# Optimization experiments

Measured on AMD Instinct MI355X. Metric: run time of the kernel, lower is better.

Reference implementation:

```python
import jax, jax.numpy as jnp
import numpy as np

B, T, C = 4, 2048, 1024
E = 8            # n_expert
K = 2            # n_expert_per_token
H = 1408         # moe_intermediate_size
HS = 1408 * 2    # shared expert intermediate (moe_intermediate_size * n_shared_expert)


def setup_inputs() -> dict:
    key = jax.random.key(0)
    k = jax.random.split(key, 8)
    s = 0.02
    return {
        "x":   jax.random.normal(k[0], (B, T, C), jnp.float32),
        "Wg":  jax.random.normal(k[1], (C, E), jnp.float32) * s,      # router gate
        "W1":  jax.random.normal(k[2], (E, C, H), jnp.float32) * s,   # fc_1 per expert
        "W2":  jax.random.normal(k[3], (E, C, H), jnp.float32) * s,   # fc_2 per expert
        "W3":  jax.random.normal(k[4], (E, H, C), jnp.float32) * s,   # proj per expert
        "Ws1": jax.random.normal(k[5], (C, HS), jnp.float32) * s,     # shared fc_1
        "Ws2": jax.random.normal(k[6], (C, HS), jnp.float32) * s,     # shared fc_2
        "Ws3": jax.random.normal(k[7], (HS, C), jnp.float32) * s,     # shared proj
    }


def reference(x, Wg, W1, W2, W3, Ws1, Ws2, Ws3):
    b, t, c = x.shape
    xf = x.reshape(-1, c)                       # [N, C]
    n = xf.shape[0]

    # Router: top-k then softmax over the selected logits (float32 softmax).
    router = xf @ Wg                            # [N, E]
    top_logits, idx = jax.lax.top_k(router, K)  # [N, K]
    probs = jax.nn.softmax(top_logits.astype(jnp.float32), axis=-1).astype(x.dtype)

    # token_expert_weights: scatter probs into dense [N, E] per-expert weights.
    w = jnp.zeros((n, E), x.dtype).at[jnp.arange(n)[:, None], idx].add(probs)

    # Per-expert gated MLP on all tokens; zero-weight tokens contribute nothing,
    # matching the masked gather/scatter-add of the original.
    h = jax.nn.silu(jnp.einsum('tc,ech->eth', xf, W1)) * jnp.einsum('tc,ech->eth', xf, W2)
    y = jnp.einsum('eth,ehc,te->tc', h, W3, w)  # weighted combine
    y = y.reshape(b, t, c)

    # Shared expert on the residual input.
    hs = jax.nn.silu(xf @ Ws1) * (xf @ Ws2)     # [N, HS]
    y = y + (hs @ Ws3).reshape(b, t, c)
    return y
```

## Files before the change

kernel.cpp:

```cpp
#include <hip/hip_runtime.h>
#include <cstdint>

#define NTOK 8192
#define CDIM 1024
#define HDIM 1408
#define HSDIM 2816
#define NEXP 8

typedef __attribute__((ext_vector_type(8))) short s8v;
typedef __attribute__((ext_vector_type(4))) float f4v;
typedef __attribute__((ext_vector_type(8))) unsigned short u16x8;

__device__ __forceinline__ unsigned short f2bf(float f) {
    unsigned int u = __float_as_uint(f);
    unsigned int r = (u + 0x7fffu + ((u >> 16) & 1u)) >> 16;
    return (unsigned short)r;
}


__global__ void cvt_bf16_kernel(const float4* __restrict__ in, ushort4* __restrict__ out, int n4) {
    int i = blockIdx.x * blockDim.x + threadIdx.x;
    if (i < n4) {
        float4 v = in[i];
        ushort4 o;
        o.x = f2bf(v.x); o.y = f2bf(v.y); o.z = f2bf(v.z); o.w = f2bf(v.w);
        out[i] = o;
    }
}

__global__ __launch_bounds__(256) void transpose_cvt_kernel(
    const float* __restrict__ in0, const float* __restrict__ in1,
    unsigned short* __restrict__ out0, unsigned short* __restrict__ out1,
    int R, int Cc, int zsplit) {
    __shared__ float T[64][68];
    int z = blockIdx.z;
    const float* in = (z < zsplit) ? in0 : in1;
    unsigned short* out = (z < zsplit) ? out0 : out1;
    int zz = (z < zsplit) ? z : z - zsplit;
    const size_t bs = (size_t)R * Cc;
    in += zz * bs; out += zz * bs;

    const int t = threadIdx.x;
    const int r0 = blockIdx.y * 64, c0 = blockIdx.x * 64;

    {
        const int rl = t >> 2, cq = t & 3;
        const float* src = in + (size_t)(r0 + rl) * Cc + c0;
#pragma unroll
        for (int i = 0; i < 4; i++) {
            float4 v = *(const float4*)(src + (cq + 4 * i) * 4);
            *(float4*)&T[rl][(cq + 4 * i) * 4] = v;
        }
    }
    __syncthreads();
    {
        const int cl = t >> 2, rq = t & 3;
        unsigned short* dst = out + (size_t)(c0 + cl) * R + r0 + rq * 16;
        u16x8 lo, hi;
#pragma unroll
        for (int j = 0; j < 8; j++) lo[j] = f2bf(T[rq * 16 + j][cl]);
#pragma unroll
        for (int j = 0; j < 8; j++) hi[j] = f2bf(T[rq * 16 + 8 + j][cl]);
        *(u16x8*)dst = lo;
        *(u16x8*)(dst + 8) = hi;
    }
}

__global__ void router_kernel(const float* __restrict__ x, const float* __restrict__ Wg,
                              int* __restrict__ idxK, float* __restrict__ probK,
                              int* __restrict__ meta) {
    int t = blockIdx.x;
    int lane = threadIdx.x;
    const float* xr = x + (size_t)t * CDIM;
    float acc[NEXP];
#pragma unroll
    for (int e = 0; e < NEXP; e++) acc[e] = 0.f;
    for (int c = lane; c < CDIM; c += 64) {
        float xv = xr[c];
        const float* wr = Wg + c * NEXP;
#pragma unroll
        for (int e = 0; e < NEXP; e++) acc[e] += xv * wr[e];
    }
#pragma unroll
    for (int e = 0; e < NEXP; e++)
        for (int off = 32; off > 0; off >>= 1)
            acc[e] += __shfl_down(acc[e], off, 64);
    if (lane == 0) {
        int b0 = 0; float v0 = acc[0];
#pragma unroll
        for (int e = 1; e < NEXP; e++) if (acc[e] > v0) { v0 = acc[e]; b0 = e; }
        int b1 = -1; float v1 = -1e30f;
#pragma unroll
        for (int e = 0; e < NEXP; e++) if (e != b0 && acc[e] > v1) { v1 = acc[e]; b1 = e; }
        float p0 = 1.f / (1.f + __expf(v1 - v0));
        idxK[2 * t] = b0; idxK[2 * t + 1] = b1;
        probK[2 * t] = p0; probK[2 * t + 1] = 1.f - p0;
        atomicAdd(&meta[b0], 1);
        atomicAdd(&meta[b1], 1);
    }
}

__global__ void offsets_kernel(int* meta) {
    int s = 0;
    for (int e = 0; e < NEXP; e++) { meta[8 + e] = s; meta[16 + e] = s; s += meta[e]; }
}

__global__ void fill_kernel(const int* __restrict__ idxK, const float* __restrict__ probK,
                            int* __restrict__ meta, int* __restrict__ rowT, float* __restrict__ rowW) {
    int t = blockIdx.x * 256 + threadIdx.x;
    if (t >= NTOK) return;
#pragma unroll
    for (int k = 0; k < 2; k++) {
        int e = idxK[2 * t + k];
        int p = atomicAdd(&meta[16 + e], 1);
        rowT[p] = t;
        rowW[p] = probK[2 * t + k];
    }
}

__global__ __launch_bounds__(256) void gemm12_kernel(
    const unsigned short* __restrict__ xb,
    const unsigned short* __restrict__ w1, const unsigned short* __restrict__ w2,
    const unsigned short* __restrict__ ws1, const unsigned short* __restrict__ ws2,
    unsigned short* __restrict__ hE, unsigned short* __restrict__ hS,
    const int* __restrict__ rowT, const int* __restrict__ meta) {
    const int id = blockIdx.x;
    int z, m0, n0; bool SH;
    if (id < 3520) { SH = false; z = id & 7; int q = id >> 3; m0 = (q % 20) * 128; n0 = (q / 20) * 64; }
    else           { SH = true;  z = 8; int q = id - 3520; m0 = (q & 63) * 128; n0 = (q >> 6) * 64; }
    const int M = SH ? NTOK : meta[z];
    const int base = SH ? 0 : meta[8 + z];
    if (m0 >= M) return;

    const unsigned short* B1 = SH ? ws1 : w1 + (size_t)z * HDIM * CDIM;
    const unsigned short* B2 = SH ? ws2 : w2 + (size_t)z * HDIM * CDIM;

    __shared__ unsigned short L[16384];

    const int tid = threadIdx.x;
    const int srow = tid >> 2;
    const int key = (tid >> 3) & 3;
    const int co = ((tid & 3) ^ key) << 3;

    int am0 = m0 + srow;       am0 = am0 < M ? am0 : M - 1;
    int am1 = m0 + 64 + srow;  am1 = am1 < M ? am1 : M - 1;
    long ar0 = SH ? am0 : rowT[base + am0];
    long ar1 = SH ? am1 : rowT[base + am1];
    const unsigned short* a0p = xb + (size_t)ar0 * CDIM + co;
    const unsigned short* a1p = xb + (size_t)ar1 * CDIM + co;
    const unsigned short* b1p = B1 + (size_t)(n0 + srow) * CDIM + co;
    const unsigned short* b2p = B2 + (size_t)(n0 + srow) * CDIM + co;

    const int w = tid >> 6, lane = tid & 63;
    const int wm = (w >> 1) * 64, wn = (w & 1) * 32;
    const int quad = lane >> 4, l15 = lane & 15;
    const int rcx = (quad ^ ((l15 >> 1) & 3)) << 3;

    f4v acc1[4][2], acc2[4][2];
#pragma unroll
    for (int i = 0; i < 4; i++)
#pragma unroll
        for (int j = 0; j < 2; j++) {
            f4v zz = {0.f, 0.f, 0.f, 0.f};
            acc1[i][j] = zz; acc2[i][j] = zz;
        }

    uint4 r0a0, r0a1, r0b1, r0b2;
    uint4 r1a0, r1a1, r1b1, r1b2;

#define LOADSET12(s, k0) do { \
        r##s##a0 = *(const uint4*)(a0p + (k0)); \
        r##s##a1 = *(const uint4*)(a1p + (k0)); \
        r##s##b1 = *(const uint4*)(b1p + (k0)); \
        r##s##b2 = *(const uint4*)(b2p + (k0)); } while (0)
#define WRITESET12(b, s) do { \
        *(uint4*)(L + (b) * 4096 + tid * 8) = r##s##a0; \
        *(uint4*)(L + (b) * 4096 + 2048 + tid * 8) = r##s##a1; \
        *(uint4*)(L + 8192 + (b) * 2048 + tid * 8) = r##s##b1; \
        *(uint4*)(L + 12288 + (b) * 2048 + tid * 8) = r##s##b2; } while (0)

    auto compute = [&](int b) {
        const unsigned short* Ab = L + b * 4096;
        const unsigned short* B1b = L + 8192 + b * 2048;
        const unsigned short* B2b = L + 12288 + b * 2048;
        s8v af[4], bf1[2], bf2[2];
#pragma unroll
        for (int mt = 0; mt < 4; mt++)
            af[mt] = *(const s8v*)(Ab + (wm + mt * 16 + l15) * 32 + rcx);
#pragma unroll
        for (int nt = 0; nt < 2; nt++) {
            bf1[nt] = *(const s8v*)(B1b + (wn + nt * 16 + l15) * 32 + rcx);
            bf2[nt] = *(const s8v*)(B2b + (wn + nt * 16 + l15) * 32 + rcx);
        }
#pragma unroll
        for (int mt = 0; mt < 4; mt++)
#pragma unroll
            for (int nt = 0; nt < 2; nt++) {
                acc1[mt][nt] = __builtin_amdgcn_mfma_f32_16x16x32_bf16(af[mt], bf1[nt], acc1[mt][nt], 0, 0, 0);
                acc2[mt][nt] = __builtin_amdgcn_mfma_f32_16x16x32_bf16(af[mt], bf2[nt], acc2[mt][nt], 0, 0, 0);
            }
    };

    const int NS = CDIM / 32;
    LOADSET12(0, 0);
    LOADSET12(1, 32);
    WRITESET12(0, 0);
    __syncthreads();
#pragma unroll 1
    for (int ks = 0; ks < NS; ks += 2) {
        if (ks + 2 < NS) LOADSET12(0, (ks + 2) * 32);
        WRITESET12(1, 1);
        compute(0);
        __syncthreads();
        if (ks + 3 < NS) LOADSET12(1, (ks + 3) * 32);
        compute(1);
        WRITESET12(0, 0);
        __syncthreads();
    }
#undef LOADSET12
#undef WRITESET12

#pragma unroll
    for (int mt = 0; mt < 4; mt++) {
#pragma unroll
        for (int r = 0; r < 4; r++) {
            int gm = m0 + wm + mt * 16 + quad * 4 + r;
            if (gm < M) {
                unsigned short* hrow = SH ? hS + (size_t)gm * HSDIM
                                          : hE + (size_t)(base + gm) * HDIM;
#pragma unroll
                for (int nt = 0; nt < 2; nt++) {
                    float z1 = acc1[mt][nt][r];
                    float z2 = acc2[mt][nt][r];
                    float hv = (z1 / (1.f + __expf(-z1))) * z2;
                    hrow[n0 + wn + nt * 16 + l15] = f2bf(hv);
                }
            }
        }
    }
}

__global__ __launch_bounds__(256) void gemm3_kernel(
    const unsigned short* __restrict__ hE, const unsigned short* __restrict__ hS,
    const unsigned short* __restrict__ w3, const unsigned short* __restrict__ ws3,
    float* __restrict__ Out,
    const int* __restrict__ rowT, const float* __restrict__ rowW, const int* __restrict__ meta) {
    const int id = blockIdx.x;
    int z, m0, n0; bool SH;
    if (id < 1280) { SH = false; z = id & 7; int q = id >> 3; m0 = (q % 20) * 128; n0 = (q / 20) * 128; }
    else           { SH = true;  z = 8; int q = id - 1280; m0 = (q & 63) * 128; n0 = (q >> 6) * 128; }
    const int M = SH ? NTOK : meta[z];
    const int base = SH ? 0 : meta[8 + z];
    if (m0 >= M) return;
    const int K = SH ? HSDIM : HDIM;
    const unsigned short* A = SH ? hS : hE;
    const unsigned short* B = SH ? ws3 : w3 + (size_t)z * CDIM * HDIM;

    __shared__ unsigned short L[16384];

    const int tid = threadIdx.x;
    const int srow = tid >> 2;
    const int key = (tid >> 3) & 3;
    const int co = ((tid & 3) ^ key) << 3;

    int am0 = m0 + srow;       am0 = am0 < M ? am0 : M - 1;
    int am1 = m0 + 64 + srow;  am1 = am1 < M ? am1 : M - 1;
    const unsigned short* a0p = A + (size_t)(base + am0) * K + co;
    const unsigned short* a1p = A + (size_t)(base + am1) * K + co;
    const unsigned short* b0p = B + (size_t)(n0 + srow) * K + co;
    const unsigned short* b1p = B + (size_t)(n0 + 64 + srow) * K + co;

    const int w = tid >> 6, lane = tid & 63;
    const int wm = (w >> 1) * 64, wn = (w & 1) * 64;
    const int quad = lane >> 4, l15 = lane & 15;
    const int rcx = (quad ^ ((l15 >> 1) & 3)) << 3;

    f4v acc[4][4];
#pragma unroll
    for (int i = 0; i < 4; i++)
#pragma unroll
        for (int j = 0; j < 4; j++) {
            f4v zz = {0.f, 0.f, 0.f, 0.f};
            acc[i][j] = zz;
        }

    uint4 r0a0, r0a1, r0b0, r0b1;
    uint4 r1a0, r1a1, r1b0, r1b1;

#define LOADSET3(s, k0) do { \
        r##s##a0 = *(const uint4*)(a0p + (k0)); \
        r##s##a1 = *(const uint4*)(a1p + (k0)); \
        r##s##b0 = *(const uint4*)(b0p + (k0)); \
        r##s##b1 = *(const uint4*)(b1p + (k0)); } while (0)
#define WRITESET3(b, s) do { \
        *(uint4*)(L + (b) * 4096 + tid * 8) = r##s##a0; \
        *(uint4*)(L + (b) * 4096 + 2048 + tid * 8) = r##s##a1; \
        *(uint4*)(L + 8192 + (b) * 4096 + tid * 8) = r##s##b0; \
        *(uint4*)(L + 8192 + (b) * 4096 + 2048 + tid * 8) = r##s##b1; } while (0)

    auto compute = [&](int b) {
        const unsigned short* Ab = L + b * 4096;
        const unsigned short* Bb = L + 8192 + b * 4096;
        s8v af[4], bf[4];
#pragma unroll
        for (int mt = 0; mt < 4; mt++)
            af[mt] = *(const s8v*)(Ab + (wm + mt * 16 + l15) * 32 + rcx);
#pragma unroll
        for (int nt = 0; nt < 4; nt++)
            bf[nt] = *(const s8v*)(Bb + (wn + nt * 16 + l15) * 32 + rcx);
#pragma unroll
        for (int mt = 0; mt < 4; mt++)
#pragma unroll
            for (int nt = 0; nt < 4; nt++)
                acc[mt][nt] = __builtin_amdgcn_mfma_f32_16x16x32_bf16(af[mt], bf[nt], acc[mt][nt], 0, 0, 0);
    };

    const int NS = K / 32;
    LOADSET3(0, 0);
    LOADSET3(1, 32);
    WRITESET3(0, 0);
    __syncthreads();
#pragma unroll 1
    for (int ks = 0; ks < NS; ks += 2) {
        if (ks + 2 < NS) LOADSET3(0, (ks + 2) * 32);
        WRITESET3(1, 1);
        compute(0);
        __syncthreads();
        if (ks + 3 < NS) LOADSET3(1, (ks + 3) * 32);
        compute(1);
        WRITESET3(0, 0);
        __syncthreads();
    }
#undef LOADSET3
#undef WRITESET3

#pragma unroll
    for (int mt = 0; mt < 4; mt++) {
#pragma unroll
        for (int r = 0; r < 4; r++) {
            int gm = m0 + wm + mt * 16 + quad * 4 + r;
            if (gm < M) {
                int t; float wgt;
                if (SH) { t = gm; wgt = 1.f; }
                else    { int rr = base + gm; t = rowT[rr]; wgt = rowW[rr]; }
                size_t o = (size_t)t * CDIM + n0 + wn + l15;
#pragma unroll
                for (int nt = 0; nt < 4; nt++)
                    atomicAdd(&Out[o + nt * 16], wgt * acc[mt][nt][r]);
            }
        }
    }
}


extern "C" void kernel_launch(void* const* d_in, const int* in_sizes, int n_in,
                              void* d_out, int out_size, void* d_ws, size_t ws_size,
                              hipStream_t stream) {
    const float* x   = (const float*)d_in[0];
    const float* Wg  = (const float*)d_in[1];
    const float* W1  = (const float*)d_in[2];
    const float* W2  = (const float*)d_in[3];
    const float* W3  = (const float*)d_in[4];
    const float* Ws1 = (const float*)d_in[5];
    const float* Ws2 = (const float*)d_in[6];
    const float* Ws3 = (const float*)d_in[7];
    float* out = (float*)d_out;

    char* p = (char*)d_ws;
    auto carve = [&](size_t bytes) {
        char* r = p;
        p += (bytes + 255) & ~(size_t)255;
        return r;
    };
    unsigned short* xb   = (unsigned short*)carve((size_t)NTOK * CDIM * 2);
    unsigned short* w1t  = (unsigned short*)carve((size_t)NEXP * HDIM * CDIM * 2);
    unsigned short* w2t  = (unsigned short*)carve((size_t)NEXP * HDIM * CDIM * 2);
    unsigned short* w3t  = (unsigned short*)carve((size_t)NEXP * CDIM * HDIM * 2);
    unsigned short* ws1t = (unsigned short*)carve((size_t)HSDIM * CDIM * 2);
    unsigned short* ws2t = (unsigned short*)carve((size_t)HSDIM * CDIM * 2);
    unsigned short* ws3t = (unsigned short*)carve((size_t)CDIM * HSDIM * 2);
    unsigned short* hE   = (unsigned short*)carve((size_t)2 * NTOK * HDIM * 2);
    unsigned short* hS   = (unsigned short*)carve((size_t)NTOK * HSDIM * 2);
    int*   idxK  = (int*)carve((size_t)NTOK * 2 * 4);
    float* probK = (float*)carve((size_t)NTOK * 2 * 4);
    int*   rowT  = (int*)carve((size_t)2 * NTOK * 4);
    float* rowW  = (float*)carve((size_t)2 * NTOK * 4);
    int*   meta  = (int*)carve(256);

    hipMemsetAsync(out, 0, (size_t)out_size * 4, stream);

    cvt_bf16_kernel<<<(NTOK * CDIM / 4 + 255) / 256, 256, 0, stream>>>(
        (const float4*)x, (ushort4*)xb, NTOK * CDIM / 4);
    transpose_cvt_kernel<<<dim3(HDIM / 64, CDIM / 64, 16), 256, 0, stream>>>(
        W1, W2, w1t, w2t, CDIM, HDIM, 8);
    transpose_cvt_kernel<<<dim3(CDIM / 64, HDIM / 64, 8), 256, 0, stream>>>(
        W3, W3, w3t, w3t, HDIM, CDIM, 8);
    transpose_cvt_kernel<<<dim3(HSDIM / 64, CDIM / 64, 2), 256, 0, stream>>>(
        Ws1, Ws2, ws1t, ws2t, CDIM, HSDIM, 1);
    transpose_cvt_kernel<<<dim3(CDIM / 64, HSDIM / 64, 1), 256, 0, stream>>>(
        Ws3, Ws3, ws3t, ws3t, HSDIM, CDIM, 1);

    hipMemsetAsync(meta, 0, 256, stream);
    router_kernel<<<NTOK, 64, 0, stream>>>(x, Wg, idxK, probK, meta);
    offsets_kernel<<<1, 1, 0, stream>>>(meta);
    fill_kernel<<<NTOK / 256, 256, 0, stream>>>(idxK, probK, meta, rowT, rowW);

    gemm12_kernel<<<3520 + 2816, 256, 0, stream>>>(
        xb, w1t, w2t, ws1t, ws2t, hE, hS, rowT, meta);
    gemm3_kernel<<<1280 + 512, 256, 0, stream>>>(
        hE, hS, w3t, ws3t, out, rowT, rowW, meta);
}
```

Measured before the change: 965.6 us.

## Replace atomic scatter-add output with plain stores plus a gather combine kernel

The down-projection GEMM no longer atomically adds weighted results into the output. The shared expert now writes its fp32 rows straight into the output, and each routed expert writes its unweighted rows as bf16 into a per-slot buffer that reuses the freed w1t/w2t workspace. A new per-token combine kernel looks up the token's two slots, applies the router weights and adds them to the output. This removes the output memset and millions of fp32 atomics, at the cost of an extra pass over the output and a bf16 rounding of the expert partials before they are combined.

```diff
diff --git a/kernel.cpp b/kernel.cpp
--- a/kernel.cpp
+++ b/kernel.cpp
@@ -15,6 +15,9 @@
     unsigned int u = __float_as_uint(f);
     unsigned int r = (u + 0x7fffu + ((u >> 16) & 1u)) >> 16;
     return (unsigned short)r;
+}
+__device__ __forceinline__ float bf2f(unsigned short u) {
+    return __uint_as_float(((unsigned int)u) << 16);
 }
 
 
@@ -106,7 +109,8 @@
 }
 
 __global__ void fill_kernel(const int* __restrict__ idxK, const float* __restrict__ probK,
-                            int* __restrict__ meta, int* __restrict__ rowT, float* __restrict__ rowW) {
+                            int* __restrict__ meta, int* __restrict__ rowT, float* __restrict__ rowW,
+                            int* __restrict__ tokSlot) {
     int t = blockIdx.x * 256 + threadIdx.x;
     if (t >= NTOK) return;
 #pragma unroll
@@ -115,6 +119,7 @@
         int p = atomicAdd(&meta[16 + e], 1);
         rowT[p] = t;
         rowW[p] = probK[2 * t + k];
+        tokSlot[2 * t + k] = p;
     }
 }
 
@@ -243,7 +248,7 @@
 __global__ __launch_bounds__(256) void gemm3_kernel(
     const unsigned short* __restrict__ hE, const unsigned short* __restrict__ hS,
     const unsigned short* __restrict__ w3, const unsigned short* __restrict__ ws3,
-    float* __restrict__ Out,
+    float* __restrict__ Out, unsigned short* __restrict__ pE,
     const int* __restrict__ rowT, const float* __restrict__ rowW, const int* __restrict__ meta) {
     const int id = blockIdx.x;
     int z, m0, n0; bool SH;
@@ -340,16 +345,38 @@
         for (int r = 0; r < 4; r++) {
             int gm = m0 + wm + mt * 16 + quad * 4 + r;
             if (gm < M) {
-                int t; float wgt;
-                if (SH) { t = gm; wgt = 1.f; }
-                else    { int rr = base + gm; t = rowT[rr]; wgt = rowW[rr]; }
-                size_t o = (size_t)t * CDIM + n0 + wn + l15;
-#pragma unroll
-                for (int nt = 0; nt < 4; nt++)
-                    atomicAdd(&Out[o + nt * 16], wgt * acc[mt][nt][r]);
+                if (SH) {
+                    size_t o = (size_t)gm * CDIM + n0 + wn + l15;
+#pragma unroll
+                    for (int nt = 0; nt < 4; nt++)
+                        Out[o + nt * 16] = acc[mt][nt][r];
+                } else {
+                    size_t o = (size_t)(base + gm) * CDIM + n0 + wn + l15;
+#pragma unroll
+                    for (int nt = 0; nt < 4; nt++)
+                        pE[o + nt * 16] = f2bf(acc[mt][nt][r]);
+                }
             }
         }
     }
+}
+
+__global__ __launch_bounds__(256) void combine_kernel(
+    float* __restrict__ Out, const unsigned short* __restrict__ pE,
+    const int* __restrict__ tokSlot, const float* __restrict__ rowW) {
+    const int t = blockIdx.x;
+    const int c = threadIdx.x * 4;
+    const int s0 = tokSlot[2 * t], s1 = tokSlot[2 * t + 1];
+    const float w0 = rowW[s0], w1 = rowW[s1];
+    float* op = Out + (size_t)t * CDIM + c;
+    float4 o = *(float4*)op;
+    ushort4 a = *(const ushort4*)(pE + (size_t)s0 * CDIM + c);
+    ushort4 b = *(const ushort4*)(pE + (size_t)s1 * CDIM + c);
+    o.x += w0 * bf2f(a.x) + w1 * bf2f(b.x);
+    o.y += w0 * bf2f(a.y) + w1 * bf2f(b.y);
+    o.z += w0 * bf2f(a.z) + w1 * bf2f(b.z);
+    o.w += w0 * bf2f(a.w) + w1 * bf2f(b.w);
+    *(float4*)op = o;
 }
 
 
@@ -381,13 +408,14 @@
     unsigned short* ws3t = (unsigned short*)carve((size_t)CDIM * HSDIM * 2);
     unsigned short* hE   = (unsigned short*)carve((size_t)2 * NTOK * HDIM * 2);
     unsigned short* hS   = (unsigned short*)carve((size_t)NTOK * HSDIM * 2);
-    int*   idxK  = (int*)carve((size_t)NTOK * 2 * 4);
-    float* probK = (float*)carve((size_t)NTOK * 2 * 4);
-    int*   rowT  = (int*)carve((size_t)2 * NTOK * 4);
-    float* rowW  = (float*)carve((size_t)2 * NTOK * 4);
-    int*   meta  = (int*)carve(256);
-
-    hipMemsetAsync(out, 0, (size_t)out_size * 4, stream);
+    int*   idxK   = (int*)carve((size_t)NTOK * 2 * 4);
+    float* probK  = (float*)carve((size_t)NTOK * 2 * 4);
+    int*   rowT   = (int*)carve((size_t)2 * NTOK * 4);
+    float* rowW   = (float*)carve((size_t)2 * NTOK * 4);
+    int*   tokSlot= (int*)carve((size_t)2 * NTOK * 4);
+    int*   meta   = (int*)carve(256);
+
+    unsigned short* pE = w1t;
 
     cvt_bf16_kernel<<<(NTOK * CDIM / 4 + 255) / 256, 256, 0, stream>>>(
         (const float4*)x, (ushort4*)xb, NTOK * CDIM / 4);
@@ -403,10 +431,11 @@
     hipMemsetAsync(meta, 0, 256, stream);
     router_kernel<<<NTOK, 64, 0, stream>>>(x, Wg, idxK, probK, meta);
     offsets_kernel<<<1, 1, 0, stream>>>(meta);
-    fill_kernel<<<NTOK / 256, 256, 0, stream>>>(idxK, probK, meta, rowT, rowW);
+    fill_kernel<<<NTOK / 256, 256, 0, stream>>>(idxK, probK, meta, rowT, rowW, tokSlot);
 
     gemm12_kernel<<<3520 + 2816, 256, 0, stream>>>(
         xb, w1t, w2t, ws1t, ws2t, hE, hS, rowT, meta);
     gemm3_kernel<<<1280 + 512, 256, 0, stream>>>(
-        hE, hS, w3t, ws3t, out, rowT, rowW, meta);
-}
+        hE, hS, w3t, ws3t, out, pE, rowT, rowW, meta);
+    combine_kernel<<<NTOK, 256, 0, stream>>>(out, pE, tokSlot, rowW);
+}
```

After: 935.6 us. 1.03x faster.
